# Optimization experiments

Measured on AMD Instinct MI355X. Metric: run time of the kernel, lower is better.

The kernel has to match this reference:

```python
import jax, jax.numpy as jnp
import numpy as np

TOKENS, IN_F, OUT_F = 8192, 4096, 4096
ZERO_POINT = 0      # input zero point (int8)
OUT_ZP = 0          # output zero point (int8)
OUT_SCALE = 0.05    # output quant scale


def setup_inputs() -> dict:
    key = jax.random.key(0)
    k1, k2, k3, k4 = jax.random.split(key, 4)
    x = jax.random.randint(k1, (TOKENS, IN_F), -128, 128, dtype=jnp.int32).astype(jnp.int8)
    # weight stored as [in_features, out_features] (module.weight.t() quantized in from_float)
    weight = jax.random.randint(k2, (IN_F, OUT_F), -127, 128, dtype=jnp.int32).astype(jnp.int8)
    bias = jax.random.randint(k3, (1, OUT_F), -1000, 1000, dtype=jnp.int32)
    gemm_scales = jax.random.uniform(k4, (1, OUT_F), minval=1e-4, maxval=2e-4, dtype=jnp.float32)
    return {"x": x, "weight": weight, "bias": bias, "gemm_scales": gemm_scales}


def reference(x, weight, bias, gemm_scales):
    # int8 -> int32 -> fp32, subtract input zero point
    a = (x.astype(jnp.int32) - ZERO_POINT).astype(jnp.float32)   # [T, IN]
    w = weight.astype(jnp.float32)                               # [IN, OUT]
    gemm_o = (a @ w + bias.astype(jnp.float32)) * gemm_scales / OUT_SCALE  # [T, OUT]
    out = jnp.clip(gemm_o + OUT_ZP, -128, 127).astype(jnp.int8)
    return out
```

## Files before the change

kernel.cpp:

```cpp
#include <hip/hip_runtime.h>
#include <stdint.h>

#define TOKENS 8192
#define IN_F   4096
#define OUT_F  4096

#define BM 128
#define BN 128
#define BK 64

typedef int v4i __attribute__((ext_vector_type(4)));

#define GLOBAL_AS __attribute__((address_space(1)))
#define LDS_AS    __attribute__((address_space(3)))

__global__ __launch_bounds__(256) void pack_x_kernel(const int* __restrict__ x32,
                                                     uint8_t* __restrict__ x8) {
  int t = blockIdx.x * 256 + threadIdx.x;
  const int4 v = ((const int4*)x32)[t];
  uint32_t p = (uint32_t)(v.x & 0xFF)
             | ((uint32_t)(v.y & 0xFF) << 8)
             | ((uint32_t)(v.z & 0xFF) << 16)
             | ((uint32_t)(v.w & 0xFF) << 24);
  ((uint32_t*)x8)[t] = p;
}

__global__ __launch_bounds__(256) void packT_w_kernel(const int* __restrict__ w32,
                                                      uint8_t* __restrict__ wt8) {
  int tn = (blockIdx.x & 63) * 64;
  int tk = (blockIdx.x >> 6) * 64;
  int t = threadIdx.x;
  int n  = tn + (t >> 2);
  int k0 = tk + (t & 3) * 16;
  uint32_t words[4];
#pragma unroll
  for (int w = 0; w < 4; ++w) {
    uint32_t acc = 0;
#pragma unroll
    for (int j = 0; j < 4; ++j) {
      int val = w32[(size_t)(k0 + w * 4 + j) * OUT_F + n];
      acc |= (uint32_t)(val & 0xFF) << (8 * j);
    }
    words[w] = acc;
  }
  uint4 o = make_uint4(words[0], words[1], words[2], words[3]);
  *(uint4*)(wt8 + (size_t)n * IN_F + k0) = o;
}

__global__ __launch_bounds__(256) void gemm_i8_kernel(const uint8_t* __restrict__ A,
                                                      const uint8_t* __restrict__ BT,
                                                      const int* __restrict__ bias,
                                                      const float* __restrict__ scales,
                                                      int* __restrict__ out) {
  __shared__ __align__(16) uint8_t As[BM * BK];
  __shared__ __align__(16) uint8_t Bs[BN * BK];

  int bid = blockIdx.x;
  int swz = (bid & 7) * 256 + (bid >> 3);
  int bm = swz >> 5;
  int bn = swz & 31;

  const int t    = threadIdx.x;
  const int lane = t & 63;
  const int w    = t >> 6;
  const int wr   = w >> 1, wc = w & 1;

  const int rowq = t >> 2;
  const int colb = (t & 3) * 16;

  const size_t aBase = (size_t)(bm * BM) * IN_F;
  const size_t bBase = (size_t)(bn * BN) * IN_F;

  v4i acc[4][4];
  const v4i vzero = {0, 0, 0, 0};
#pragma unroll
  for (int i = 0; i < 4; ++i)
#pragma unroll
    for (int j = 0; j < 4; ++j) acc[i][j] = vzero;

  const int fr   = lane & 15;
  const int fq   = lane >> 4;
  const int aoff = fq * 16;

  for (int k0 = 0; k0 < IN_F; k0 += BK) {
#pragma unroll
    for (int i = 0; i < 2; ++i) {
      const uint8_t* ga = A + aBase + (size_t)(i * 64 + rowq) * IN_F + k0 + colb;
      __builtin_amdgcn_global_load_lds((const GLOBAL_AS void*)ga,
                                       (LDS_AS void*)(As + i * 4096 + t * 16),
                                       16, 0, 0);
      const uint8_t* gb = BT + bBase + (size_t)(i * 64 + rowq) * IN_F + k0 + colb;
      __builtin_amdgcn_global_load_lds((const GLOBAL_AS void*)gb,
                                       (LDS_AS void*)(Bs + i * 4096 + t * 16),
                                       16, 0, 0);
    }
    __syncthreads();

    v4i af[4], bf[4];
#pragma unroll
    for (int m = 0; m < 4; ++m)
      af[m] = *(const v4i*)(As + (wr * 64 + m * 16 + fr) * BK + aoff);
#pragma unroll
    for (int n = 0; n < 4; ++n)
      bf[n] = *(const v4i*)(Bs + (wc * 64 + n * 16 + fr) * BK + aoff);
#pragma unroll
    for (int m = 0; m < 4; ++m)
#pragma unroll
      for (int n = 0; n < 4; ++n)
        acc[m][n] = __builtin_amdgcn_mfma_i32_16x16x64_i8(af[m], bf[n], acc[m][n], 0, 0, 0);
    __syncthreads();
  }

#pragma unroll
  for (int n = 0; n < 4; ++n) {
    const int gn  = bn * BN + wc * 64 + n * 16 + fr;
    const int bsv = bias[gn];
    const float sc = scales[gn] * 20.0f;
#pragma unroll
    for (int m = 0; m < 4; ++m) {
      const int gm0 = bm * BM + wr * 64 + m * 16 + fq * 4;
#pragma unroll
      for (int r = 0; r < 4; ++r) {
        float g = (float)(acc[m][n][r] + bsv) * sc;
        g = fminf(fmaxf(g, -128.0f), 127.0f);
        out[(size_t)(gm0 + r) * OUT_F + gn] = (int)g;
      }
    }
  }
}

extern "C" void kernel_launch(void* const* d_in, const int* in_sizes, int n_in,
                              void* d_out, int out_size, void* d_ws, size_t ws_size,
                              hipStream_t stream) {
  const int*   x32    = (const int*)d_in[0];
  const int*   w32    = (const int*)d_in[1];
  const int*   bias   = (const int*)d_in[2];
  const float* scales = (const float*)d_in[3];
  int* out = (int*)d_out;

  uint8_t* x8  = (uint8_t*)d_ws;
  uint8_t* wt8 = (uint8_t*)d_ws + (size_t)TOKENS * IN_F;

  pack_x_kernel<<<(TOKENS * IN_F / 4) / 256, 256, 0, stream>>>(x32, x8);
  packT_w_kernel<<<(OUT_F / 64) * (IN_F / 64), 256, 0, stream>>>(w32, wt8);
  gemm_i8_kernel<<<(TOKENS / BM) * (OUT_F / BN), 256, 0, stream>>>(x8, wt8, bias, scales, out);
}
```

Before: 226.2 us.

## Use 256x256 tiles with 4-stage LDS pipeline, swizzled layout and 8 waves

Grows the GEMM tile to 256x256 with 512 threads and adds a 4-deep ring of LDS buffers. Direct-to-LDS global loads are issued three stages ahead, with explicit vmcnt waits and a single barrier per k-step. LDS rows are XOR-swizzled to reduce bank conflicts, and s_setprio is raised around the MFMA bursts. This targets global-load latency and barrier stalls and gives more data reuse per tile. In exchange it uses 128KB of LDS and 128 accumulator registers per thread, which limits occupancy.

```diff
diff --git a/kernel.cpp b/kernel.cpp
--- a/kernel.cpp
+++ b/kernel.cpp
@@ -5,9 +5,11 @@
 #define IN_F   4096
 #define OUT_F  4096
 
-#define BM 128
-#define BN 128
+#define BM 256
+#define BN 256
 #define BK 64
+#define NK (IN_F / BK)
+#define THREADS 512
 
 typedef int v4i __attribute__((ext_vector_type(4)));
 
@@ -47,69 +49,114 @@
   *(uint4*)(wt8 + (size_t)n * IN_F + k0) = o;
 }
 
-__global__ __launch_bounds__(256) void gemm_i8_kernel(const uint8_t* __restrict__ A,
-                                                      const uint8_t* __restrict__ BT,
-                                                      const int* __restrict__ bias,
-                                                      const float* __restrict__ scales,
-                                                      int* __restrict__ out) {
-  __shared__ __align__(16) uint8_t As[BM * BK];
-  __shared__ __align__(16) uint8_t Bs[BN * BK];
-
-  int bid = blockIdx.x;
-  int swz = (bid & 7) * 256 + (bid >> 3);
-  int bm = swz >> 5;
-  int bn = swz & 31;
+__global__ __launch_bounds__(THREADS, 2) void gemm_i8_kernel(const uint8_t* __restrict__ A,
+                                                             const uint8_t* __restrict__ BT,
+                                                             const int* __restrict__ bias,
+                                                             const float* __restrict__ scales,
+                                                             int* __restrict__ out) {
+  __shared__ __align__(16) uint8_t lds[4 * 32768];
 
   const int t    = threadIdx.x;
   const int lane = t & 63;
   const int w    = t >> 6;
-  const int wr   = w >> 1, wc = w & 1;
+  const int wr   = w >> 2;
+  const int wc   = w & 3;
+  const int fr   = lane & 15;
+  const int fq   = lane >> 4;
 
-  const int rowq = t >> 2;
-  const int colb = (t & 3) * 16;
+  int bid = blockIdx.x;
+  int swz = (bid & 7) * 64 + (bid >> 3);
+  int bm = swz >> 4;
+  int bn = swz & 15;
 
-  const size_t aBase = (size_t)(bm * BM) * IN_F;
-  const size_t bBase = (size_t)(bn * BN) * IN_F;
+  const int lsz  = t ^ ((t >> 3) & 7);
+  const int srow = lsz >> 2;
+  const int scol = (lsz & 3) * 16;
+  const size_t gA0 = (size_t)(bm * BM + srow) * IN_F + scol;
+  const size_t gA1 = gA0 + (size_t)128 * IN_F;
+  const size_t gB0 = (size_t)(bn * BN + srow) * IN_F + scol;
+  const size_t gB1 = gB0 + (size_t)128 * IN_F;
+  const int ldst = t * 16;
 
-  v4i acc[4][4];
+  auto stage = [&](int j) {
+    uint8_t* sb = lds + (j & 3) * 32768;
+    const int k0 = j * BK;
+    __builtin_amdgcn_global_load_lds((const GLOBAL_AS void*)(A  + gA0 + k0),
+                                     (LDS_AS void*)(sb + ldst),           16, 0, 0);
+    __builtin_amdgcn_global_load_lds((const GLOBAL_AS void*)(A  + gA1 + k0),
+                                     (LDS_AS void*)(sb + 8192  + ldst),   16, 0, 0);
+    __builtin_amdgcn_global_load_lds((const GLOBAL_AS void*)(BT + gB0 + k0),
+                                     (LDS_AS void*)(sb + 16384 + ldst),   16, 0, 0);
+    __builtin_amdgcn_global_load_lds((const GLOBAL_AS void*)(BT + gB1 + k0),
+                                     (LDS_AS void*)(sb + 24576 + ldst),   16, 0, 0);
+  };
+
+  int aoff[8], boff[4];
+#pragma unroll
+  for (int m = 0; m < 8; ++m) {
+    int row = wr * 128 + m * 16 + fr;
+    int half = row >> 7, rl = row & 127;
+    int b = rl * 64 + fq * 16;
+    b ^= ((rl >> 1) & 7) << 4;
+    aoff[m] = half * 8192 + b;
+  }
+#pragma unroll
+  for (int n = 0; n < 4; ++n) {
+    int row = wc * 64 + n * 16 + fr;
+    int half = row >> 7, rl = row & 127;
+    int b = rl * 64 + fq * 16;
+    b ^= ((rl >> 1) & 7) << 4;
+    boff[n] = 16384 + half * 8192 + b;
+  }
+
+  v4i acc[8][4];
   const v4i vzero = {0, 0, 0, 0};
 #pragma unroll
-  for (int i = 0; i < 4; ++i)
+  for (int m = 0; m < 8; ++m)
 #pragma unroll
-    for (int j = 0; j < 4; ++j) acc[i][j] = vzero;
+    for (int n = 0; n < 4; ++n) acc[m][n] = vzero;
 
-  const int fr   = lane & 15;
-  const int fq   = lane >> 4;
-  const int aoff = fq * 16;
-
-  for (int k0 = 0; k0 < IN_F; k0 += BK) {
+  auto compute = [&](int i) {
+    const uint8_t* sb = lds + (i & 3) * 32768;
+    v4i bf[4], af[4];
 #pragma unroll
-    for (int i = 0; i < 2; ++i) {
-      const uint8_t* ga = A + aBase + (size_t)(i * 64 + rowq) * IN_F + k0 + colb;
-      __builtin_amdgcn_global_load_lds((const GLOBAL_AS void*)ga,
-                                       (LDS_AS void*)(As + i * 4096 + t * 16),
-                                       16, 0, 0);
-      const uint8_t* gb = BT + bBase + (size_t)(i * 64 + rowq) * IN_F + k0 + colb;
-      __builtin_amdgcn_global_load_lds((const GLOBAL_AS void*)gb,
-                                       (LDS_AS void*)(Bs + i * 4096 + t * 16),
-                                       16, 0, 0);
-    }
-    __syncthreads();
-
-    v4i af[4], bf[4];
+    for (int n = 0; n < 4; ++n) bf[n] = *(const v4i*)(sb + boff[n]);
 #pragma unroll
-    for (int m = 0; m < 4; ++m)
-      af[m] = *(const v4i*)(As + (wr * 64 + m * 16 + fr) * BK + aoff);
-#pragma unroll
-    for (int n = 0; n < 4; ++n)
-      bf[n] = *(const v4i*)(Bs + (wc * 64 + n * 16 + fr) * BK + aoff);
+    for (int m = 0; m < 4; ++m) af[m] = *(const v4i*)(sb + aoff[m]);
+    __builtin_amdgcn_s_setprio(1);
 #pragma unroll
     for (int m = 0; m < 4; ++m)
 #pragma unroll
       for (int n = 0; n < 4; ++n)
         acc[m][n] = __builtin_amdgcn_mfma_i32_16x16x64_i8(af[m], bf[n], acc[m][n], 0, 0, 0);
-    __syncthreads();
+    __builtin_amdgcn_s_setprio(0);
+#pragma unroll
+    for (int m = 0; m < 4; ++m) af[m] = *(const v4i*)(sb + aoff[4 + m]);
+    __builtin_amdgcn_s_setprio(1);
+#pragma unroll
+    for (int m = 0; m < 4; ++m)
+#pragma unroll
+      for (int n = 0; n < 4; ++n)
+        acc[4 + m][n] = __builtin_amdgcn_mfma_i32_16x16x64_i8(af[m], bf[n], acc[4 + m][n], 0, 0, 0);
+    __builtin_amdgcn_s_setprio(0);
+  };
+
+  stage(0); stage(1); stage(2);
+
+#define ITER(i, VM, DOSTAGE)                                       \
+  asm volatile("s_waitcnt vmcnt(" #VM ")" ::: "memory");           \
+  asm volatile("s_barrier" ::: "memory");                          \
+  if (DOSTAGE) stage((i) + 3);                                     \
+  __builtin_amdgcn_sched_barrier(0);                               \
+  compute(i);
+
+  for (int i = 0; i < NK - 3; ++i) {
+    ITER(i, 8, true)
   }
+  ITER(NK - 3, 8, false)
+  ITER(NK - 2, 4, false)
+  ITER(NK - 1, 0, false)
+#undef ITER
 
 #pragma unroll
   for (int n = 0; n < 4; ++n) {
@@ -117,8 +164,8 @@
     const int bsv = bias[gn];
     const float sc = scales[gn] * 20.0f;
 #pragma unroll
-    for (int m = 0; m < 4; ++m) {
-      const int gm0 = bm * BM + wr * 64 + m * 16 + fq * 4;
+    for (int m = 0; m < 8; ++m) {
+      const int gm0 = bm * BM + wr * 128 + m * 16 + fq * 4;
 #pragma unroll
       for (int r = 0; r < 4; ++r) {
         float g = (float)(acc[m][n][r] + bsv) * sc;
@@ -143,5 +190,5 @@
 
   pack_x_kernel<<<(TOKENS * IN_F / 4) / 256, 256, 0, stream>>>(x32, x8);
   packT_w_kernel<<<(OUT_F / 64) * (IN_F / 64), 256, 0, stream>>>(w32, wt8);
-  gemm_i8_kernel<<<(TOKENS / BM) * (OUT_F / BN), 256, 0, stream>>>(x8, wt8, bias, scales, out);
+  gemm_i8_kernel<<<(TOKENS / BM) * (OUT_F / BN), THREADS, 0, stream>>>(x8, wt8, bias, scales, out);
 }
```

New measurement: 194.8 us. 13.9% less time.
